# Kernel tuning notes

Hardware: AMD Instinct MI355X
Metric: run time of the kernel (lower is better)

Reference implementation:

```python
import jax, jax.numpy as jnp
import numpy as np

N, D = 65536, 1024  # points, in_dim == out_dim (required by the module's double use of linear.weight)


def setup_inputs() -> dict:
    key = jax.random.key(0)
    k_x, k_w, k_W, k_noise = jax.random.split(key, 4)
    x = jax.random.normal(k_x, (N, D), dtype=jnp.float32)
    w = jax.random.normal(k_w, (D,), dtype=jnp.float32)  # style vector (len == in_dim)
    # learned params of nn.Linear(in_dim, out_dim)
    W = jax.random.normal(k_W, (D, D), dtype=jnp.float32) * 0.02  # [out_dim, in_dim]
    b = jnp.zeros((D,), dtype=jnp.float32)
    # noise path: torch does randn(1, out_dim) * noise_strength each forward;
    # we materialize the raw noise deterministically for reproducibility.
    noise_strength = jnp.full((1,), 0.1, dtype=jnp.float32)
    noise_raw = jax.random.normal(k_noise, (1, D), dtype=jnp.float32)
    return {"x": x, "w": w, "W": W, "b": b,
            "noise_strength": noise_strength, "noise_raw": noise_raw}


def reference(x, w, W, b, noise_strength, noise_raw):
    # 1) plain linear: x1 = x @ W.T + b            [N, D]
    x1 = x @ W.T + b
    # 2) modulated_linear(x1, W, styles=w, noise, demodulate=True)
    #    demod coefficients: rsqrt(sum_j (W[o,j]*w[j])^2 + 1e-8)   [D]
    dcoefs = jax.lax.rsqrt(jnp.sum(jnp.square(W * w[None, :]), axis=1) + 1e-8)
    #    modulate input, dense matmul with raw weight
    x2 = (x1 * w) @ W.T                            # [N, D]
    #    fma: x2 * dcoefs + noise
    noise = noise_raw * noise_strength             # [1, D]
    x3 = x2 * dcoefs[None, :] + noise
    # 3) bias add + leaky_relu (torch default negative_slope=0.01)
    return jax.nn.leaky_relu(x3 + b, negative_slope=0.01)
```

## Files before the change

kernel.cpp:

```cpp
#include <hip/hip_runtime.h>
#include <hip/hip_bf16.h>

using bf16 = __hip_bfloat16;
typedef __attribute__((ext_vector_type(8))) short bf16x8;
typedef __attribute__((ext_vector_type(4))) float f32x4;

#define DDIM 1024

__device__ __forceinline__ void gload16(const bf16* g, bf16* l) {
    __builtin_amdgcn_global_load_lds(
        (const __attribute__((address_space(1))) void*)g,
        (__attribute__((address_space(3))) void*)l, 16, 0, 0);
}
__device__ __forceinline__ short f2b(float f) {
    return (short)__bfloat16_as_ushort(__float2bfloat16(f));
}


__global__ void prep_kernel(const float* __restrict__ W, const float* __restrict__ w,
                            const float* __restrict__ b, const float* __restrict__ nstr,
                            const float* __restrict__ nraw,
                            float* __restrict__ dco, float* __restrict__ add,
                            bf16* __restrict__ Qb) {
    int o = blockIdx.x;
    int lane = threadIdx.x;
    const float* Wrow = W + (size_t)o * DDIM;
    bf16* Qrow = Qb + (size_t)o * DDIM;
    float s = 0.f, c = 0.f;
    for (int j = lane; j < DDIM; j += 64) {
        float q = Wrow[j] * w[j];
        Qrow[j] = __float2bfloat16(q);
        s += q * q;
        c += b[j] * q;
    }
#pragma unroll
    for (int off = 32; off; off >>= 1) {
        s += __shfl_down(s, off);
        c += __shfl_down(c, off);
    }
    if (lane == 0) {
        float d = rsqrtf(s + 1e-8f);
        dco[o] = d;
        add[o] = c * d + nraw[o] * nstr[0] + b[o];
    }
}

__global__ void transpose_kernel(const float* __restrict__ W, bf16* __restrict__ Wt) {
    __shared__ bf16 tile[64][72];
    int bi = blockIdx.x * 64;
    int bj = blockIdx.y * 64;
    int r  = threadIdx.x >> 2;
    int c4 = (threadIdx.x & 3) * 16;
    const float* src = W + (size_t)(bi + r) * DDIM + bj + c4;
#pragma unroll
    for (int i = 0; i < 16; ++i) tile[r][c4 + i] = __float2bfloat16(src[i]);
    __syncthreads();
    bf16* dst = Wt + (size_t)(bj + r) * DDIM + bi + c4;
#pragma unroll
    for (int i = 0; i < 16; ++i) dst[i] = tile[c4 + i][r];
}

__global__ __launch_bounds__(256) void mgemm(const bf16* __restrict__ A,
                                             const bf16* __restrict__ B,
                                             bf16* __restrict__ C) {
    __shared__ bf16 lA[128 * 32];
    __shared__ bf16 lB[128 * 32];
    int tid  = threadIdx.x;
    int lane = tid & 63, wid = tid >> 6;
    int wr = wid >> 1, wc = wid & 1;
    int brow = blockIdx.x >> 3;
    int bcol = blockIdx.x & 7;
    const bf16* Ab = A + (size_t)brow * 128 * DDIM;
    const bf16* Bb = B + (size_t)bcol * 128 * DDIM;
    int srow = tid >> 2;
    int scol = (tid & 3) * 8;
    f32x4 acc[4][4];
#pragma unroll
    for (int m = 0; m < 4; ++m)
#pragma unroll
        for (int n = 0; n < 4; ++n) acc[m][n] = (f32x4){0.f, 0.f, 0.f, 0.f};
    int r16 = lane & 15, kh = lane >> 4;
    for (int k0 = 0; k0 < DDIM; k0 += 32) {
        gload16(Ab + (size_t)srow * DDIM + k0 + scol,        lA + tid * 8);
        gload16(Ab + (size_t)(srow + 64) * DDIM + k0 + scol, lA + (tid + 256) * 8);
        gload16(Bb + (size_t)srow * DDIM + k0 + scol,        lB + tid * 8);
        gload16(Bb + (size_t)(srow + 64) * DDIM + k0 + scol, lB + (tid + 256) * 8);
        __syncthreads();
        bf16x8 aF[4], bF[4];
#pragma unroll
        for (int m = 0; m < 4; ++m) {
            aF[m] = *(const bf16x8*)(lA + ((wr * 64 + m * 16 + r16) * 32 + kh * 8));
            bF[m] = *(const bf16x8*)(lB + ((wc * 64 + m * 16 + r16) * 32 + kh * 8));
        }
#pragma unroll
        for (int m = 0; m < 4; ++m)
#pragma unroll
            for (int n = 0; n < 4; ++n)
                acc[m][n] = __builtin_amdgcn_mfma_f32_16x16x32_bf16(aF[m], bF[n], acc[m][n], 0, 0, 0);
        __syncthreads();
    }
    int cb = lane & 15;
    int rb = (lane >> 4) * 4;
#pragma unroll
    for (int n = 0; n < 4; ++n) {
        int col = bcol * 128 + wc * 64 + n * 16 + cb;
#pragma unroll
        for (int m = 0; m < 4; ++m)
#pragma unroll
            for (int j = 0; j < 4; ++j) {
                int row = wr * 64 + m * 16 + rb + j;
                C[((size_t)brow * 128 + row) * DDIM + col] = __float2bfloat16(acc[m][n][j]);
            }
    }
}

#define BAR()  __builtin_amdgcn_s_barrier()
#define VMW(n) asm volatile("s_waitcnt vmcnt(" #n ")")
#define LGW()  asm volatile("s_waitcnt lgkmcnt(0)")

__global__ __launch_bounds__(512, 2) void big_gemm(
    const float* __restrict__ Af, const bf16* __restrict__ Bw,
    const float* __restrict__ dco, const float* __restrict__ add,
    float* __restrict__ Cf)
{
    __shared__ bf16 sA[2][2][256 * 32];
    __shared__ bf16 sB[2][2][256 * 32];

    const int tid  = threadIdx.x;
    const int lane = tid & 63;
    const int wid  = tid >> 6;
    const int wr   = wid >> 2, wc = wid & 3;
    const int r16  = lane & 15, kh = lane >> 4;
    const int fso  = (kh ^ ((r16 >> 1) & 3)) * 8;

    int bx  = blockIdx.x;
    int swz = (bx & 7) * 128 + (bx >> 3);
    int brow = swz >> 2, bcol = swz & 3;

    const float* Asrc_f = Af + (size_t)(brow * 256) * DDIM;
    const bf16*  Bsrc   = Bw + (size_t)(bcol * 256) * DDIM;

    const int sr  = tid >> 2;
    const int ssl = (tid & 3) ^ ((sr >> 1) & 3);

    f32x4 acc[8][4];
#pragma unroll
    for (int m = 0; m < 8; ++m)
#pragma unroll
        for (int n = 0; n < 4; ++n) acc[m][n] = (f32x4){0.f, 0.f, 0.f, 0.f};

    bf16x8 aF[4], aF2[4], bF[4];
    float4 gA0, gA1, gA2, gA3;
    float4 gB0, gB1, gB2, gB3;

#define STAGE_B(buf, kt, ks) do { \
    const bf16* _s = Bsrc + (size_t)sr * DDIM + ((kt) * 64 + (ks) * 32 + ssl * 8); \
    gload16(_s,               &sB[buf][ks][tid * 8]); \
    gload16(_s + 128 * DDIM,  &sB[buf][ks][(tid + 512) * 8]); \
} while (0)

#define LOAD_A_F(g0, g1, g2, g3, kt, ks) do { \
    const float* _p = Asrc_f + (size_t)sr * DDIM + ((kt) * 64 + (ks) * 32 + (tid & 3) * 8); \
    g0 = ((const float4*)_p)[0]; g1 = ((const float4*)_p)[1]; \
    const float* _q = _p + 128 * DDIM; \
    g2 = ((const float4*)_q)[0]; g3 = ((const float4*)_q)[1]; \
} while (0)

#define WRITE_A(buf, ks, g0, g1, g2, g3) do { \
    bf16x8 _pk; \
    _pk[0]=f2b(g0.x); _pk[1]=f2b(g0.y); _pk[2]=f2b(g0.z); _pk[3]=f2b(g0.w); \
    _pk[4]=f2b(g1.x); _pk[5]=f2b(g1.y); _pk[6]=f2b(g1.z); _pk[7]=f2b(g1.w); \
    *(bf16x8*)&sA[buf][ks][sr * 32 + ssl * 8] = _pk; \
    _pk[0]=f2b(g2.x); _pk[1]=f2b(g2.y); _pk[2]=f2b(g2.z); _pk[3]=f2b(g2.w); \
    _pk[4]=f2b(g3.x); _pk[5]=f2b(g3.y); _pk[6]=f2b(g3.z); _pk[7]=f2b(g3.w); \
    *(bf16x8*)&sA[buf][ks][(sr + 128) * 32 + ssl * 8] = _pk; \
} while (0)

#define RD_A(dst, buf, ks, mh) do { \
    _Pragma("unroll") for (int _m = 0; _m < 4; ++_m) \
        dst[_m] = *(const bf16x8*)&sA[buf][ks][(wr * 128 + (mh) * 64 + _m * 16 + r16) * 32 + fso]; \
} while (0)

#define RD_B(buf, ks) do { \
    _Pragma("unroll") for (int _n = 0; _n < 4; ++_n) \
        bF[_n] = *(const bf16x8*)&sB[buf][ks][(wc * 64 + _n * 16 + r16) * 32 + fso]; \
} while (0)

#define MFMA32() do { \
    __builtin_amdgcn_s_setprio(1); \
    _Pragma("unroll") for (int _m = 0; _m < 4; ++_m) { \
        acc[_m][0] = __builtin_amdgcn_mfma_f32_16x16x32_bf16(aF[_m], bF[0], acc[_m][0], 0, 0, 0); \
        acc[_m][1] = __builtin_amdgcn_mfma_f32_16x16x32_bf16(aF[_m], bF[1], acc[_m][1], 0, 0, 0); \
        acc[_m][2] = __builtin_amdgcn_mfma_f32_16x16x32_bf16(aF[_m], bF[2], acc[_m][2], 0, 0, 0); \
        acc[_m][3] = __builtin_amdgcn_mfma_f32_16x16x32_bf16(aF[_m], bF[3], acc[_m][3], 0, 0, 0); \
    } \
    _Pragma("unroll") for (int _m = 0; _m < 4; ++_m) { \
        acc[4+_m][0] = __builtin_amdgcn_mfma_f32_16x16x32_bf16(aF2[_m], bF[0], acc[4+_m][0], 0, 0, 0); \
        acc[4+_m][1] = __builtin_amdgcn_mfma_f32_16x16x32_bf16(aF2[_m], bF[1], acc[4+_m][1], 0, 0, 0); \
        acc[4+_m][2] = __builtin_amdgcn_mfma_f32_16x16x32_bf16(aF2[_m], bF[2], acc[4+_m][2], 0, 0, 0); \
        acc[4+_m][3] = __builtin_amdgcn_mfma_f32_16x16x32_bf16(aF2[_m], bF[3], acc[4+_m][3], 0, 0, 0); \
    } \
    __builtin_amdgcn_s_setprio(0); \
} while (0)

    LOAD_A_F(gA0, gA1, gA2, gA3, 0, 0);
    LOAD_A_F(gB0, gB1, gB2, gB3, 0, 1);
    STAGE_B(0, 0, 0);
    STAGE_B(0, 0, 1);
    VMW(8);
    WRITE_A(0, 0, gA0, gA1, gA2, gA3);
    VMW(4);
    WRITE_A(0, 1, gB0, gB1, gB2, gB3);
    LOAD_A_F(gA0, gA1, gA2, gA3, 1, 0);
    LOAD_A_F(gB0, gB1, gB2, gB3, 1, 1);
    LGW();
    VMW(8);
    BAR();

    for (int t = 0; t < 16; ++t) {
        int b = t & 1, nb = b ^ 1;
        int t1 = t + 1; if (t1 > 15) t1 = 15;
        int t2 = t + 2; if (t2 > 15) t2 = 15;

        RD_A(aF,  b, 0, 0);
        RD_A(aF2, b, 0, 1);
        RD_B(b, 0);
        VMW(4);
        WRITE_A(nb, 0, gA0, gA1, gA2, gA3);
        STAGE_B(nb, t1, 0);
        STAGE_B(nb, t1, 1);
        LGW();
        BAR();
        MFMA32();
        BAR();

        RD_A(aF,  b, 1, 0);
        RD_A(aF2, b, 1, 1);
        RD_B(b, 1);
        VMW(4);
        WRITE_A(nb, 1, gB0, gB1, gB2, gB3);
        LOAD_A_F(gA0, gA1, gA2, gA3, t2, 0);
        LOAD_A_F(gB0, gB1, gB2, gB3, t2, 1);
        LGW();
        BAR();
        MFMA32();
        VMW(8);
        BAR();
    }

    int crb = brow * 256 + wr * 128 + kh * 4;
    int ccb = bcol * 256 + wc * 64 + r16;
#pragma unroll
    for (int n = 0; n < 4; ++n) {
        int col = ccb + n * 16;
        float cm = dco[col], ca = add[col];
#pragma unroll
        for (int m = 0; m < 8; ++m) {
#pragma unroll
            for (int j = 0; j < 4; ++j) {
                size_t idx = (size_t)(crb + m * 16 + j) * DDIM + col;
                float v = acc[m][n][j] * cm + ca;
                v = (v >= 0.f) ? v : 0.01f * v;
                Cf[idx] = v;
            }
        }
    }
#undef STAGE_B
#undef LOAD_A_F
#undef WRITE_A
#undef RD_A
#undef RD_B
#undef MFMA32
}

extern "C" void kernel_launch(void* const* d_in, const int* in_sizes, int n_in,
                              void* d_out, int out_size, void* d_ws, size_t ws_size,
                              hipStream_t stream) {
    const float* x  = (const float*)d_in[0];
    const float* w  = (const float*)d_in[1];
    const float* W  = (const float*)d_in[2];
    const float* b  = (const float*)d_in[3];
    const float* ns = (const float*)d_in[4];
    const float* nr = (const float*)d_in[5];
    float* out = (float*)d_out;

    float* dco = (float*)d_ws;
    float* add = dco + DDIM;
    bf16*  Qb  = (bf16*)((char*)d_ws + 8192);
    bf16*  Wt  = (bf16*)((char*)d_ws + 8192 + 2097152);
    bf16*  Mt  = (bf16*)((char*)d_ws + 8192 + 2 * 2097152);

    int M = in_sizes[0] / DDIM;
    int grid = (M / 256) * (DDIM / 256);

    prep_kernel<<<DDIM, 64, 0, stream>>>(W, w, b, ns, nr, dco, add, Qb);
    transpose_kernel<<<dim3(16, 16), 256, 0, stream>>>(W, Wt);
    mgemm<<<64, 256, 0, stream>>>(Qb, Wt, Mt);
    big_gemm<<<grid, 512, 0, stream>>>(x, Mt, dco, add, out);
}
```

Measured before the change: 273.3 us.

## Pre-convert x to bf16 in separate kernel and stage A via direct LDS loads

Adds a standalone kernel that converts the fp32 input x to bf16 in workspace, then has the big GEMM load A tiles with global_load_lds, as it already does for B, instead of loading fp32 into registers and converting in-loop. The main loop is simplified to one barrier per K-step, with both K-halves' fragments read up front. This removes per-thread conversion work and register pressure from the GEMM. In exchange it adds an extra pass over x: a 256MB read plus a 128MB write and re-read. Workspace is reused by aliasing xb with Qb after mgemm consumes it.

Result: slower. 316.1 us (+15.7%).

```diff
diff --git a/kernel.cpp b/kernel.cpp
--- a/kernel.cpp
+++ b/kernel.cpp
@@ -114,12 +114,24 @@
     }
 }
 
+__global__ __launch_bounds__(256) void convert_kernel(const float* __restrict__ x,
+                                                      bf16* __restrict__ xb, int n8) {
+    int stride = gridDim.x * blockDim.x;
+    for (int i = blockIdx.x * blockDim.x + threadIdx.x; i < n8; i += stride) {
+        const float4* p = (const float4*)(x + (size_t)i * 8);
+        float4 v0 = p[0], v1 = p[1];
+        bf16x8 pk;
+        pk[0]=f2b(v0.x); pk[1]=f2b(v0.y); pk[2]=f2b(v0.z); pk[3]=f2b(v0.w);
+        pk[4]=f2b(v1.x); pk[5]=f2b(v1.y); pk[6]=f2b(v1.z); pk[7]=f2b(v1.w);
+        *(bf16x8*)(xb + (size_t)i * 8) = pk;
+    }
+}
+
 #define BAR()  __builtin_amdgcn_s_barrier()
 #define VMW(n) asm volatile("s_waitcnt vmcnt(" #n ")")
-#define LGW()  asm volatile("s_waitcnt lgkmcnt(0)")
 
 __global__ __launch_bounds__(512, 2) void big_gemm(
-    const float* __restrict__ Af, const bf16* __restrict__ Bw,
+    const bf16* __restrict__ Ab, const bf16* __restrict__ Bw,
     const float* __restrict__ dco, const float* __restrict__ add,
     float* __restrict__ Cf)
 {
@@ -137,8 +149,8 @@
     int swz = (bx & 7) * 128 + (bx >> 3);
     int brow = swz >> 2, bcol = swz & 3;
 
-    const float* Asrc_f = Af + (size_t)(brow * 256) * DDIM;
-    const bf16*  Bsrc   = Bw + (size_t)(bcol * 256) * DDIM;
+    const bf16* Asrc = Ab + (size_t)(brow * 256) * DDIM;
+    const bf16* Bsrc = Bw + (size_t)(bcol * 256) * DDIM;
 
     const int sr  = tid >> 2;
     const int ssl = (tid & 3) ^ ((sr >> 1) & 3);
@@ -150,8 +162,13 @@
         for (int n = 0; n < 4; ++n) acc[m][n] = (f32x4){0.f, 0.f, 0.f, 0.f};
 
     bf16x8 aF[4], aF2[4], bF[4];
-    float4 gA0, gA1, gA2, gA3;
-    float4 gB0, gB1, gB2, gB3;
+    bf16x8 cF[4], cF2[4], dF[4];
+
+#define STAGE_A(buf, kt, ks) do { \
+    const bf16* _s = Asrc + (size_t)sr * DDIM + ((kt) * 64 + (ks) * 32 + ssl * 8); \
+    gload16(_s,               &sA[buf][ks][tid * 8]); \
+    gload16(_s + 128 * DDIM,  &sA[buf][ks][(tid + 512) * 8]); \
+} while (0)
 
 #define STAGE_B(buf, kt, ks) do { \
     const bf16* _s = Bsrc + (size_t)sr * DDIM + ((kt) * 64 + (ks) * 32 + ssl * 8); \
@@ -159,92 +176,52 @@
     gload16(_s + 128 * DDIM,  &sB[buf][ks][(tid + 512) * 8]); \
 } while (0)
 
-#define LOAD_A_F(g0, g1, g2, g3, kt, ks) do { \
-    const float* _p = Asrc_f + (size_t)sr * DDIM + ((kt) * 64 + (ks) * 32 + (tid & 3) * 8); \
-    g0 = ((const float4*)_p)[0]; g1 = ((const float4*)_p)[1]; \
-    const float* _q = _p + 128 * DDIM; \
-    g2 = ((const float4*)_q)[0]; g3 = ((const float4*)_q)[1]; \
-} while (0)
-
-#define WRITE_A(buf, ks, g0, g1, g2, g3) do { \
-    bf16x8 _pk; \
-    _pk[0]=f2b(g0.x); _pk[1]=f2b(g0.y); _pk[2]=f2b(g0.z); _pk[3]=f2b(g0.w); \
-    _pk[4]=f2b(g1.x); _pk[5]=f2b(g1.y); _pk[6]=f2b(g1.z); _pk[7]=f2b(g1.w); \
-    *(bf16x8*)&sA[buf][ks][sr * 32 + ssl * 8] = _pk; \
-    _pk[0]=f2b(g2.x); _pk[1]=f2b(g2.y); _pk[2]=f2b(g2.z); _pk[3]=f2b(g2.w); \
-    _pk[4]=f2b(g3.x); _pk[5]=f2b(g3.y); _pk[6]=f2b(g3.z); _pk[7]=f2b(g3.w); \
-    *(bf16x8*)&sA[buf][ks][(sr + 128) * 32 + ssl * 8] = _pk; \
-} while (0)
-
 #define RD_A(dst, buf, ks, mh) do { \
     _Pragma("unroll") for (int _m = 0; _m < 4; ++_m) \
         dst[_m] = *(const bf16x8*)&sA[buf][ks][(wr * 128 + (mh) * 64 + _m * 16 + r16) * 32 + fso]; \
 } while (0)
 
-#define RD_B(buf, ks) do { \
+#define RD_B(dst, buf, ks) do { \
     _Pragma("unroll") for (int _n = 0; _n < 4; ++_n) \
-        bF[_n] = *(const bf16x8*)&sB[buf][ks][(wc * 64 + _n * 16 + r16) * 32 + fso]; \
-} while (0)
-
-#define MFMA32() do { \
+        dst[_n] = *(const bf16x8*)&sB[buf][ks][(wc * 64 + _n * 16 + r16) * 32 + fso]; \
+} while (0)
+
+#define MFMA32(A0, A1, B) do { \
     __builtin_amdgcn_s_setprio(1); \
     _Pragma("unroll") for (int _m = 0; _m < 4; ++_m) { \
-        acc[_m][0] = __builtin_amdgcn_mfma_f32_16x16x32_bf16(aF[_m], bF[0], acc[_m][0], 0, 0, 0); \
-        acc[_m][1] = __builtin_amdgcn_mfma_f32_16x16x32_bf16(aF[_m], bF[1], acc[_m][1], 0, 0, 0); \
-        acc[_m][2] = __builtin_amdgcn_mfma_f32_16x16x32_bf16(aF[_m], bF[2], acc[_m][2], 0, 0, 0); \
-        acc[_m][3] = __builtin_amdgcn_mfma_f32_16x16x32_bf16(aF[_m], bF[3], acc[_m][3], 0, 0, 0); \
+        acc[_m][0] = __builtin_amdgcn_mfma_f32_16x16x32_bf16(A0[_m], B[0], acc[_m][0], 0, 0, 0); \
+        acc[_m][1] = __builtin_amdgcn_mfma_f32_16x16x32_bf16(A0[_m], B[1], acc[_m][1], 0, 0, 0); \
+        acc[_m][2] = __builtin_amdgcn_mfma_f32_16x16x32_bf16(A0[_m], B[2], acc[_m][2], 0, 0, 0); \
+        acc[_m][3] = __builtin_amdgcn_mfma_f32_16x16x32_bf16(A0[_m], B[3], acc[_m][3], 0, 0, 0); \
     } \
     _Pragma("unroll") for (int _m = 0; _m < 4; ++_m) { \
-        acc[4+_m][0] = __builtin_amdgcn_mfma_f32_16x16x32_bf16(aF2[_m], bF[0], acc[4+_m][0], 0, 0, 0); \
-        acc[4+_m][1] = __builtin_amdgcn_mfma_f32_16x16x32_bf16(aF2[_m], bF[1], acc[4+_m][1], 0, 0, 0); \
-        acc[4+_m][2] = __builtin_amdgcn_mfma_f32_16x16x32_bf16(aF2[_m], bF[2], acc[4+_m][2], 0, 0, 0); \
-        acc[4+_m][3] = __builtin_amdgcn_mfma_f32_16x16x32_bf16(aF2[_m], bF[3], acc[4+_m][3], 0, 0, 0); \
+        acc[4+_m][0] = __builtin_amdgcn_mfma_f32_16x16x32_bf16(A1[_m], B[0], acc[4+_m][0], 0, 0, 0); \
+        acc[4+_m][1] = __builtin_amdgcn_mfma_f32_16x16x32_bf16(A1[_m], B[1], acc[4+_m][1], 0, 0, 0); \
+        acc[4+_m][2] = __builtin_amdgcn_mfma_f32_16x16x32_bf16(A1[_m], B[2], acc[4+_m][2], 0, 0, 0); \
+        acc[4+_m][3] = __builtin_amdgcn_mfma_f32_16x16x32_bf16(A1[_m], B[3], acc[4+_m][3], 0, 0, 0); \
     } \
     __builtin_amdgcn_s_setprio(0); \
 } while (0)
 
-    LOAD_A_F(gA0, gA1, gA2, gA3, 0, 0);
-    LOAD_A_F(gB0, gB1, gB2, gB3, 0, 1);
-    STAGE_B(0, 0, 0);
-    STAGE_B(0, 0, 1);
-    VMW(8);
-    WRITE_A(0, 0, gA0, gA1, gA2, gA3);
-    VMW(4);
-    WRITE_A(0, 1, gB0, gB1, gB2, gB3);
-    LOAD_A_F(gA0, gA1, gA2, gA3, 1, 0);
-    LOAD_A_F(gB0, gB1, gB2, gB3, 1, 1);
-    LGW();
-    VMW(8);
+    STAGE_A(0, 0, 0); STAGE_A(0, 0, 1);
+    STAGE_B(0, 0, 0); STAGE_B(0, 0, 1);
+    VMW(0);
     BAR();
 
     for (int t = 0; t < 16; ++t) {
         int b = t & 1, nb = b ^ 1;
         int t1 = t + 1; if (t1 > 15) t1 = 15;
-        int t2 = t + 2; if (t2 > 15) t2 = 15;
-
-        RD_A(aF,  b, 0, 0);
-        RD_A(aF2, b, 0, 1);
-        RD_B(b, 0);
-        VMW(4);
-        WRITE_A(nb, 0, gA0, gA1, gA2, gA3);
-        STAGE_B(nb, t1, 0);
-        STAGE_B(nb, t1, 1);
-        LGW();
-        BAR();
-        MFMA32();
-        BAR();
-
-        RD_A(aF,  b, 1, 0);
-        RD_A(aF2, b, 1, 1);
-        RD_B(b, 1);
-        VMW(4);
-        WRITE_A(nb, 1, gB0, gB1, gB2, gB3);
-        LOAD_A_F(gA0, gA1, gA2, gA3, t2, 0);
-        LOAD_A_F(gB0, gB1, gB2, gB3, t2, 1);
-        LGW();
-        BAR();
-        MFMA32();
-        VMW(8);
+
+        RD_A(aF,  b, 0, 0); RD_A(aF2, b, 0, 1); RD_B(bF, b, 0);
+        RD_A(cF,  b, 1, 0); RD_A(cF2, b, 1, 1); RD_B(dF, b, 1);
+
+        STAGE_A(nb, t1, 0); STAGE_A(nb, t1, 1);
+        STAGE_B(nb, t1, 0); STAGE_B(nb, t1, 1);
+
+        MFMA32(aF, aF2, bF);
+        MFMA32(cF, cF2, dF);
+
+        VMW(0);
         BAR();
     }
 
@@ -265,9 +242,8 @@
             }
         }
     }
+#undef STAGE_A
 #undef STAGE_B
-#undef LOAD_A_F
-#undef WRITE_A
 #undef RD_A
 #undef RD_B
 #undef MFMA32
@@ -286,9 +262,10 @@
 
     float* dco = (float*)d_ws;
     float* add = dco + DDIM;
-    bf16*  Qb  = (bf16*)((char*)d_ws + 8192);
-    bf16*  Wt  = (bf16*)((char*)d_ws + 8192 + 2097152);
-    bf16*  Mt  = (bf16*)((char*)d_ws + 8192 + 2 * 2097152);
+    bf16*  Mt  = (bf16*)((char*)d_ws + 8192);
+    bf16*  Qb  = (bf16*)((char*)d_ws + 8192 + 2097152);
+    bf16*  Wt  = (bf16*)((char*)d_ws + 8192 + 2 * 2097152);
+    bf16*  xb  = (bf16*)((char*)d_ws + 8192 + 2097152);
 
     int M = in_sizes[0] / DDIM;
     int grid = (M / 256) * (DDIM / 256);
@@ -296,5 +273,6 @@
     prep_kernel<<<DDIM, 64, 0, stream>>>(W, w, b, ns, nr, dco, add, Qb);
     transpose_kernel<<<dim3(16, 16), 256, 0, stream>>>(W, Wt);
     mgemm<<<64, 256, 0, stream>>>(Qb, Wt, Mt);
-    big_gemm<<<grid, 512, 0, stream>>>(x, Mt, dco, add, out);
-}
+    convert_kernel<<<2048, 256, 0, stream>>>(x, xb, M * DDIM / 8);
+    big_gemm<<<grid, 512, 0, stream>>>(xb, Mt, dco, add, out);
+}
```

## Read both k-halves up front and use one barrier per main-loop iteration

Applied to the files above, without the earlier changes.

The main GEMM loop now loads the A and B fragments for both k-sub-steps from LDS at the start of each iteration, into extra fragment registers. It then writes the converted A tile and issues the B and next-A global loads before running both MFMA blocks back to back. This cuts the loop from four barriers per iteration to one and lets the global loads overlap a longer stretch of MFMA work. The cost is 48 more VGPRs for fragments on top of the 128 accumulator registers, which risks spills or lower occupancy. It also adds a full vmcnt(0) drain before the second A write.

After: 317.8 us. +16.3%, slower.

```diff
diff --git a/kernel.cpp b/kernel.cpp
--- a/kernel.cpp
+++ b/kernel.cpp
@@ -150,6 +150,7 @@
         for (int n = 0; n < 4; ++n) acc[m][n] = (f32x4){0.f, 0.f, 0.f, 0.f};
 
     bf16x8 aF[4], aF2[4], bF[4];
+    bf16x8 cF[4], cF2[4], dF[4];
     float4 gA0, gA1, gA2, gA3;
     float4 gB0, gB1, gB2, gB3;
 
@@ -181,36 +182,35 @@
         dst[_m] = *(const bf16x8*)&sA[buf][ks][(wr * 128 + (mh) * 64 + _m * 16 + r16) * 32 + fso]; \
 } while (0)
 
-#define RD_B(buf, ks) do { \
+#define RD_B(dst, buf, ks) do { \
     _Pragma("unroll") for (int _n = 0; _n < 4; ++_n) \
-        bF[_n] = *(const bf16x8*)&sB[buf][ks][(wc * 64 + _n * 16 + r16) * 32 + fso]; \
-} while (0)
-
-#define MFMA32() do { \
+        dst[_n] = *(const bf16x8*)&sB[buf][ks][(wc * 64 + _n * 16 + r16) * 32 + fso]; \
+} while (0)
+
+#define MFMA32(A0, A1, B) do { \
     __builtin_amdgcn_s_setprio(1); \
     _Pragma("unroll") for (int _m = 0; _m < 4; ++_m) { \
-        acc[_m][0] = __builtin_amdgcn_mfma_f32_16x16x32_bf16(aF[_m], bF[0], acc[_m][0], 0, 0, 0); \
-        acc[_m][1] = __builtin_amdgcn_mfma_f32_16x16x32_bf16(aF[_m], bF[1], acc[_m][1], 0, 0, 0); \
-        acc[_m][2] = __builtin_amdgcn_mfma_f32_16x16x32_bf16(aF[_m], bF[2], acc[_m][2], 0, 0, 0); \
-        acc[_m][3] = __builtin_amdgcn_mfma_f32_16x16x32_bf16(aF[_m], bF[3], acc[_m][3], 0, 0, 0); \
+        acc[_m][0] = __builtin_amdgcn_mfma_f32_16x16x32_bf16(A0[_m], B[0], acc[_m][0], 0, 0, 0); \
+        acc[_m][1] = __builtin_amdgcn_mfma_f32_16x16x32_bf16(A0[_m], B[1], acc[_m][1], 0, 0, 0); \
+        acc[_m][2] = __builtin_amdgcn_mfma_f32_16x16x32_bf16(A0[_m], B[2], acc[_m][2], 0, 0, 0); \
+        acc[_m][3] = __builtin_amdgcn_mfma_f32_16x16x32_bf16(A0[_m], B[3], acc[_m][3], 0, 0, 0); \
     } \
     _Pragma("unroll") for (int _m = 0; _m < 4; ++_m) { \
-        acc[4+_m][0] = __builtin_amdgcn_mfma_f32_16x16x32_bf16(aF2[_m], bF[0], acc[4+_m][0], 0, 0, 0); \
-        acc[4+_m][1] = __builtin_amdgcn_mfma_f32_16x16x32_bf16(aF2[_m], bF[1], acc[4+_m][1], 0, 0, 0); \
-        acc[4+_m][2] = __builtin_amdgcn_mfma_f32_16x16x32_bf16(aF2[_m], bF[2], acc[4+_m][2], 0, 0, 0); \
-        acc[4+_m][3] = __builtin_amdgcn_mfma_f32_16x16x32_bf16(aF2[_m], bF[3], acc[4+_m][3], 0, 0, 0); \
+        acc[4+_m][0] = __builtin_amdgcn_mfma_f32_16x16x32_bf16(A1[_m], B[0], acc[4+_m][0], 0, 0, 0); \
+        acc[4+_m][1] = __builtin_amdgcn_mfma_f32_16x16x32_bf16(A1[_m], B[1], acc[4+_m][1], 0, 0, 0); \
+        acc[4+_m][2] = __builtin_amdgcn_mfma_f32_16x16x32_bf16(A1[_m], B[2], acc[4+_m][2], 0, 0, 0); \
+        acc[4+_m][3] = __builtin_amdgcn_mfma_f32_16x16x32_bf16(A1[_m], B[3], acc[4+_m][3], 0, 0, 0); \
     } \
     __builtin_amdgcn_s_setprio(0); \
 } while (0)
 
     LOAD_A_F(gA0, gA1, gA2, gA3, 0, 0);
     LOAD_A_F(gB0, gB1, gB2, gB3, 0, 1);
-    STAGE_B(0, 0, 0);
-    STAGE_B(0, 0, 1);
-    VMW(8);
+    VMW(4);
     WRITE_A(0, 0, gA0, gA1, gA2, gA3);
-    VMW(4);
+    VMW(0);
     WRITE_A(0, 1, gB0, gB1, gB2, gB3);
+    STAGE_B(0, 0, 0); STAGE_B(0, 0, 1);
     LOAD_A_F(gA0, gA1, gA2, gA3, 1, 0);
     LOAD_A_F(gB0, gB1, gB2, gB3, 1, 1);
     LGW();
@@ -222,28 +222,22 @@
         int t1 = t + 1; if (t1 > 15) t1 = 15;
         int t2 = t + 2; if (t2 > 15) t2 = 15;
 
-        RD_A(aF,  b, 0, 0);
-        RD_A(aF2, b, 0, 1);
-        RD_B(b, 0);
+        RD_A(aF,  b, 0, 0); RD_A(aF2, b, 0, 1); RD_B(bF, b, 0);
+        RD_A(cF,  b, 1, 0); RD_A(cF2, b, 1, 1); RD_B(dF, b, 1);
+
         VMW(4);
         WRITE_A(nb, 0, gA0, gA1, gA2, gA3);
-        STAGE_B(nb, t1, 0);
-        STAGE_B(nb, t1, 1);
-        LGW();
-        BAR();
-        MFMA32();
-        BAR();
-
-        RD_A(aF,  b, 1, 0);
-        RD_A(aF2, b, 1, 1);
-        RD_B(b, 1);
-        VMW(4);
+        VMW(0);
         WRITE_A(nb, 1, gB0, gB1, gB2, gB3);
+
+        STAGE_B(nb, t1, 0); STAGE_B(nb, t1, 1);
         LOAD_A_F(gA0, gA1, gA2, gA3, t2, 0);
         LOAD_A_F(gB0, gB1, gB2, gB3, t2, 1);
+
+        MFMA32(aF, aF2, bF);
+        MFMA32(cF, cF2, dF);
+
         LGW();
-        BAR();
-        MFMA32();
         VMW(8);
         BAR();
     }
```
